# Kernel optimization log

Measured on AMD Instinct MI355X. Metric: run time of the kernel, lower is better.

Reference implementation:

```python
import jax, jax.numpy as jnp
import numpy as np

DIM = 2048
NUM_HEADS = 16
NUM_KV_HEADS = 4
HEAD_DIM = DIM // NUM_HEADS  # 128
ROPE_BASE = 10000.0
BATCH = 2
SEQLEN = 2048


def _rms_norm(x):
    # F.rms_norm over last dim, no weight; torch default eps = dtype eps
    eps = jnp.finfo(x.dtype).eps
    ms = jnp.mean(jnp.square(x), axis=-1, keepdims=True)
    return x * jax.lax.rsqrt(ms + eps)


def _rotary_cos_sin(seqlen, dtype):
    # Rotary(head_dim, base): inv_freq over even indices, freqs = t outer inv_freq
    inv_freq = 1.0 / (ROPE_BASE ** (jnp.arange(0, HEAD_DIM, 2, dtype=jnp.float32) / HEAD_DIM))
    t = jnp.arange(seqlen, dtype=jnp.float32)
    freqs = jnp.outer(t, inv_freq)  # [T, HEAD_DIM//2]
    return jnp.cos(freqs).astype(dtype), jnp.sin(freqs).astype(dtype)


def _apply_rotary_emb(x, cos, sin):
    # x: [B, H, T, D]; split halves (modded-nanogpt style)
    d = x.shape[-1] // 2
    x1, x2 = x[..., :d], x[..., d:]
    y1 = x1 * cos + x2 * sin
    y2 = -x1 * sin + x2 * cos
    return jnp.concatenate([y1, y2], axis=-1)


def setup_inputs() -> dict:
    key = jax.random.key(0)
    ks = jax.random.split(key, 6)
    kv_dim = NUM_KV_HEADS * HEAD_DIM
    s_in = 1.0 / np.sqrt(DIM)
    return {
        "x": jax.random.normal(ks[0], (BATCH, SEQLEN, DIM), dtype=jnp.float32),
        "q_gain": jax.random.uniform(ks[1], (NUM_HEADS,), dtype=jnp.float32, minval=0.5, maxval=1.5),
        "W_q": jax.random.normal(ks[2], (DIM, DIM), dtype=jnp.float32) * s_in,
        "W_k": jax.random.normal(ks[3], (kv_dim, DIM), dtype=jnp.float32) * s_in,
        "W_v": jax.random.normal(ks[4], (kv_dim, DIM), dtype=jnp.float32) * s_in,
        "W_proj": jax.random.normal(ks[5], (DIM, DIM), dtype=jnp.float32) * s_in,
    }


def reference(x, q_gain, W_q, W_k, W_v, W_proj):
    B, T, D = x.shape
    # QKV projections (Linear with weight [out, in])
    q = (x @ W_q.T).reshape(B, T, NUM_HEADS, HEAD_DIM).transpose(0, 2, 1, 3)   # [B,H,T,d]
    k = (x @ W_k.T).reshape(B, T, NUM_KV_HEADS, HEAD_DIM).transpose(0, 2, 1, 3)
    v = (x @ W_v.T).reshape(B, T, NUM_KV_HEADS, HEAD_DIM).transpose(0, 2, 1, 3)
    # dual RMSNorm on q/k
    q = _rms_norm(q)
    k = _rms_norm(k)
    # RoPE
    cos, sin = _rotary_cos_sin(T, q.dtype)
    q = _apply_rotary_emb(q, cos, sin)
    k = _apply_rotary_emb(k, cos, sin)
    # per-head gain on q
    q = q * q_gain.astype(q.dtype)[None, :, None, None]
    # GQA: repeat kv heads to match query heads
    g = NUM_HEADS // NUM_KV_HEADS
    k = jnp.repeat(k, g, axis=1)
    v = jnp.repeat(v, g, axis=1)
    # causal scaled dot product attention
    scale = 1.0 / np.sqrt(HEAD_DIM)
    scores = jnp.einsum('bhqd,bhkd->bhqk', q, k) * scale
    causal = jnp.tril(jnp.ones((T, T), dtype=bool))
    scores = jnp.where(causal[None, None], scores, jnp.finfo(scores.dtype).min)
    probs = jax.nn.softmax(scores, axis=-1)
    y = jnp.einsum('bhqk,bhkd->bhqd', probs, v)  # [B,H,T,d]
    y = y.transpose(0, 2, 1, 3).reshape(B, T, D)
    return y @ W_proj.T
```

## Files before the change

### kernel.cpp

```cpp
#include <hip/hip_runtime.h>
#include <hip/hip_bf16.h>
#include <type_traits>

#define DIMN   2048
#define NH     16
#define NKVH   4
#define HD     128
#define KVD    512
#define NQKV   3072
#define BATCH  2
#define SEQ    2048
#define MROWS  4096
#define VOFF   2560

typedef __attribute__((ext_vector_type(8))) __bf16 bf16x8;
typedef __attribute__((ext_vector_type(4))) float floatx4;

#define BIG_NEG (-1.0e30f)

__device__ __forceinline__ short bf16rn(float f) {
  union { __bf16 h; short s; } u;
  u.h = (__bf16)f;
  return u.s;
}
__device__ __forceinline__ float bf2f(short s) {
  union { unsigned u; float f; } v;
  v.u = ((unsigned)(unsigned short)s) << 16;
  return v.f;
}

__device__ __forceinline__ void async_cp16(const short* g, short* l) {
  __builtin_amdgcn_global_load_lds(
      (const __attribute__((address_space(1))) unsigned int*)g,
      (__attribute__((address_space(3))) unsigned int*)l, 16, 0, 0);
}

__global__ void f32_to_bf16_kern(const float* __restrict__ in,
                                 short* __restrict__ out, int n8) {
  int i = blockIdx.x * blockDim.x + threadIdx.x;
  if (i >= n8) return;
  float4 a = ((const float4*)in)[i * 2];
  float4 b = ((const float4*)in)[i * 2 + 1];
  short r[8];
  r[0] = bf16rn(a.x); r[1] = bf16rn(a.y); r[2] = bf16rn(a.z); r[3] = bf16rn(a.w);
  r[4] = bf16rn(b.x); r[5] = bf16rn(b.y); r[6] = bf16rn(b.z); r[7] = bf16rn(b.w);
  ((uint4*)out)[i] = *(const uint4*)r;
}

template <typename OUT>
__global__ __launch_bounds__(256) void gemm_bt_as(const short* __restrict__ A,
                                                  const short* __restrict__ Bw,
                                                  OUT* __restrict__ C,
                                                  int N, int K) {
  __shared__ __align__(16) short As[2][128 * 32];
  __shared__ __align__(16) short Bs[2][128 * 32];
  const int t = threadIdx.x;
  const int lane = t & 63, wave = t >> 6;
  const int lrow = lane & 15, quad = lane >> 4;
  const int wr = wave >> 1, wc = wave & 1;
  const int m0 = blockIdx.y * 128, n0 = blockIdx.x * 128;

  const short* pa[2];
  const short* pb[2];
  int wi2[2];
#pragma unroll
  for (int i = 0; i < 2; i++) {
    int wi = wave * 2 + i;
    int row = wi * 16 + (lane >> 2);
    int col = ((lane & 3) ^ (row & 3)) * 8;
    pa[i] = A + (size_t)(m0 + row) * K + col;
    pb[i] = Bw + (size_t)(n0 + row) * K + col;
    wi2[i] = wi;
  }

  floatx4 acc[4][4] = {};
  const int iters = K >> 5;

#pragma unroll
  for (int i = 0; i < 2; i++) {
    async_cp16(pa[i], &As[0][wi2[i] * 512]);
    async_cp16(pb[i], &Bs[0][wi2[i] * 512]);
  }

  for (int it = 0; it < iters; it++) {
    const int cur = it & 1;
    __syncthreads();

    if (it + 1 < iters) {
      const int off = (it + 1) * 32;
#pragma unroll
      for (int i = 0; i < 2; i++) {
        async_cp16(pa[i] + off, &As[cur ^ 1][wi2[i] * 512]);
        async_cp16(pb[i] + off, &Bs[cur ^ 1][wi2[i] * 512]);
      }
    }

    bf16x8 af[4], bfr[4];
#pragma unroll
    for (int mt = 0; mt < 4; mt++) {
      int row = wr * 64 + mt * 16 + lrow;
      af[mt] = *(const bf16x8*)&As[cur][row * 32 + (quad ^ (lrow & 3)) * 8];
    }
#pragma unroll
    for (int nt = 0; nt < 4; nt++) {
      int row = wc * 64 + nt * 16 + lrow;
      bfr[nt] = *(const bf16x8*)&Bs[cur][row * 32 + (quad ^ (lrow & 3)) * 8];
    }
#pragma unroll
    for (int mt = 0; mt < 4; mt++)
#pragma unroll
      for (int nt = 0; nt < 4; nt++)
        acc[mt][nt] = __builtin_amdgcn_mfma_f32_16x16x32_bf16(af[mt], bfr[nt],
                                                              acc[mt][nt], 0, 0, 0);
  }

#pragma unroll
  for (int mt = 0; mt < 4; mt++)
#pragma unroll
    for (int nt = 0; nt < 4; nt++) {
      int row = m0 + wr * 64 + mt * 16 + quad * 4;
      int col = n0 + wc * 64 + nt * 16 + lrow;
#pragma unroll
      for (int r = 0; r < 4; r++) {
        if constexpr (std::is_same<OUT, short>::value)
          C[(size_t)(row + r) * N + col] = bf16rn(acc[mt][nt][r]);
        else
          C[(size_t)(row + r) * N + col] = acc[mt][nt][r];
      }
    }
}

__global__ __launch_bounds__(256) void rms_rope_kern(const short* __restrict__ qkv,
                                                     const float* __restrict__ gain,
                                                     short* __restrict__ qb,
                                                     short* __restrict__ kb) {
  const int t = threadIdx.x;
  const int lane = t & 63, wave = t >> 6;
  const int gw = blockIdx.x * 4 + wave;
  const int row = gw / 20, slot = gw - row * 20;
  const int pos = row & (SEQ - 1);

  const short* src = (slot < 16) ? qkv + (size_t)row * NQKV + slot * HD
                                 : qkv + (size_t)row * NQKV + DIMN + (slot - 16) * HD;
  float x1 = bf2f(src[lane]), x2 = bf2f(src[lane + 64]);

  float ss = x1 * x1 + x2 * x2;
#pragma unroll
  for (int off = 32; off > 0; off >>= 1) ss += __shfl_xor(ss, off);
  float inv = rsqrtf(ss * (1.0f / 128.0f) + 1.1920928955078125e-7f);
  x1 *= inv; x2 *= inv;
  float fr = (float)pos * exp2f((float)lane * -0.20762050593045935f);
  float s, c;
  sincosf(fr, &s, &c);
  float y1 = x1 * c + x2 * s;
  float y2 = x2 * c - x1 * s;
  if (slot < 16) {
    float g = gain[slot] * 0.12751744459132754f;
    y1 *= g; y2 *= g;
  }
  short o1 = bf16rn(y1), o2 = bf16rn(y2);
  if (slot < 16) { short* d = qb + (size_t)row * DIMN + slot * HD;        d[lane] = o1; d[lane + 64] = o2; }
  else           { short* d = kb + (size_t)row * KVD + (slot - 16) * HD;  d[lane] = o1; d[lane + 64] = o2; }
}

__global__ __launch_bounds__(256) void vT_kern(const short* __restrict__ qkv,
                                               short* __restrict__ vT) {
  __shared__ short L[64 * 68];
  const int t0 = blockIdx.x * 64, d0 = blockIdx.y * 64;
  const int b = blockIdx.z >> 2, kvh = blockIdx.z & 3;
  const int t = threadIdx.x;

#pragma unroll
  for (int p = 0; p < 4; p++) {
    int tt = p * 16 + (t >> 4);
    int dd = (t & 15) * 4;
    ushort4 v = *(const ushort4*)(qkv + (size_t)(b * SEQ + t0 + tt) * NQKV + VOFF + kvh * HD + d0 + dd);
    *(ushort4*)&L[tt * 68 + dd] = v;
  }
  __syncthreads();

  const int dl = t >> 2;
  const int tc = (t & 3) * 16;
  short tmp[16];
#pragma unroll
  for (int j = 0; j < 16; j++) tmp[j] = L[(tc + j) * 68 + dl];
  size_t obase = (size_t)((b * NKVH + kvh) * HD + d0 + dl) * SEQ + t0 + tc;
  *(uint4*)(vT + obase)     = ((const uint4*)tmp)[0];
  *(uint4*)(vT + obase + 8) = ((const uint4*)tmp)[1];
}

__global__ __launch_bounds__(256) void attn_kern(const short* __restrict__ qb,
                                                 const short* __restrict__ kb,
                                                 const short* __restrict__ vT,
                                                 short* __restrict__ yb) {
  __shared__ __align__(16) short Ks[2][64 * 128];
  __shared__ __align__(16) short Vs[128 * 64];
  __shared__ __align__(16) short Ps[64 * 72];
  const int qp = blockIdx.x;
  const int g  = blockIdx.y;
  const int b = g >> 4, h = g & 15, kvh = h >> 2;
  const int t = threadIdx.x, lane = t & 63, wave = t >> 6;
  const int lrow = lane & 15, quad = lane >> 4;

  int k_row[4], k_col[4], v_row[4], v_col[4];
#pragma unroll
  for (int i = 0; i < 4; i++) {
    int wi = wave * 4 + i;
    int kr = wi * 4 + (lane >> 4);
    k_row[i] = kr; k_col[i] = ((lane & 15) ^ (kr & 7)) * 8;
    int vr = wi * 8 + (lane >> 3);
    v_row[i] = vr; v_col[i] = ((lane & 7) ^ (vr & 7)) * 8;
  }
  const short* kbase = kb + (size_t)b * SEQ * KVD + kvh * HD;
  const short* vbase = vT + (size_t)(b * NKVH + kvh) * HD * SEQ;

  bf16x8 vones;
#pragma unroll
  for (int j = 0; j < 8; j++) vones[j] = (__bf16)1.0f;

  for (int ph = 0; ph < 2; ph++) {
    const int qt = ph ? (31 - qp) : qp;
    const int q0 = qt * 64;

    __syncthreads();

    bf16x8 aq[4];
    const short* qrow = qb + (size_t)(b * SEQ + q0 + wave * 16 + lrow) * DIMN + h * HD;
#pragma unroll
    for (int kk = 0; kk < 4; kk++)
      aq[kk] = *(const bf16x8*)(qrow + kk * 32 + quad * 8);

    floatx4 O[8] = {};
    floatx4 Ol = {};
    float mI[4];
#pragma unroll
    for (int r = 0; r < 4; r++) mI[r] = BIG_NEG;

#pragma unroll
    for (int i = 0; i < 4; i++)
      async_cp16(kbase + (size_t)k_row[i] * KVD + k_col[i], &Ks[0][(wave * 4 + i) * 512]);

    for (int kt = 0; kt <= qt; kt++) {
      const int cur = kt & 1;
      const int k0 = kt * 64;
      __syncthreads();

#pragma unroll
      for (int i = 0; i < 4; i++)
        async_cp16(vbase + (size_t)v_row[i] * SEQ + k0 + v_col[i], &Vs[(wave * 4 + i) * 512]);
      if (kt < qt) {
        const int kn = k0 + 64;
#pragma unroll
        for (int i = 0; i < 4; i++)
          async_cp16(kbase + (size_t)(kn + k_row[i]) * KVD + k_col[i],
                     &Ks[cur ^ 1][(wave * 4 + i) * 512]);
      }

      floatx4 S[4] = {};
#pragma unroll
      for (int kk = 0; kk < 4; kk++)
#pragma unroll
        for (int nt = 0; nt < 4; nt++) {
          int row = nt * 16 + lrow;
          bf16x8 bk = *(const bf16x8*)&Ks[cur][row * 128 + ((kk * 4 + quad) ^ (row & 7)) * 8];
          S[nt] = __builtin_amdgcn_mfma_f32_16x16x32_bf16(aq[kk], bk, S[nt], 0, 0, 0);
        }

      if (kt == qt) {
#pragma unroll
        for (int nt = 0; nt < 4; nt++) {
          int kj = nt * 16 + lrow;
#pragma unroll
          for (int r = 0; r < 4; r++) {
            int qi = wave * 16 + quad * 4 + r;
            if (kj > qi) S[nt][r] = BIG_NEG;
          }
        }
      }

#pragma unroll
      for (int r = 0; r < 4; r++) {
        float mx = fmaxf(fmaxf(S[0][r], S[1][r]), fmaxf(S[2][r], S[3][r]));
        mx = fmaxf(mx, __shfl_xor(mx, 1));
        mx = fmaxf(mx, __shfl_xor(mx, 2));
        mx = fmaxf(mx, __shfl_xor(mx, 4));
        mx = fmaxf(mx, __shfl_xor(mx, 8));
        if (!__all(mx <= mI[r] + 8.0f)) {
          float mNew = fmaxf(mI[r], mx);
          float alpha = exp2f(mI[r] - mNew);
          mI[r] = mNew;
#pragma unroll
          for (int n2 = 0; n2 < 8; n2++) O[n2][r] *= alpha;
          Ol[r] *= alpha;
        }
#pragma unroll
        for (int nt = 0; nt < 4; nt++) S[nt][r] = exp2f(S[nt][r] - mI[r]);
      }

#pragma unroll
      for (int nt = 0; nt < 4; nt++) {
        int cwr = ((nt * 2 + (lrow >> 3)) ^ (quad * 2)) * 8 + (lrow & 7);
#pragma unroll
        for (int r = 0; r < 4; r++)
          Ps[(wave * 16 + quad * 4 + r) * 72 + cwr] = bf16rn(S[nt][r]);
      }

      __syncthreads();

#pragma unroll
      for (int kk = 0; kk < 2; kk++) {
        int capc = ((kk * 4 + quad) ^ (2 * ((lrow >> 2) & 3))) * 8;
        bf16x8 ap = *(const bf16x8*)&Ps[(wave * 16 + lrow) * 72 + capc];
#pragma unroll
        for (int n2 = 0; n2 < 8; n2++) {
          int row = n2 * 16 + lrow;
          bf16x8 bv = *(const bf16x8*)&Vs[row * 64 + ((kk * 4 + quad) ^ (row & 7)) * 8];
          O[n2] = __builtin_amdgcn_mfma_f32_16x16x32_bf16(ap, bv, O[n2], 0, 0, 0);
        }
        Ol = __builtin_amdgcn_mfma_f32_16x16x32_bf16(ap, vones, Ol, 0, 0, 0);
      }
    }

    float il[4];
#pragma unroll
    for (int r = 0; r < 4; r++) il[r] = 1.0f / Ol[r];
#pragma unroll
    for (int n2 = 0; n2 < 8; n2++)
#pragma unroll
      for (int r = 0; r < 4; r++) {
        float val = O[n2][r] * il[r];
        int row = q0 + wave * 16 + quad * 4 + r;
        int col = h * HD + n2 * 16 + lrow;
        yb[(size_t)(b * SEQ + row) * DIMN + col] = bf16rn(val);
      }
  }
}

extern "C" void kernel_launch(void* const* d_in, const int* in_sizes, int n_in,
                              void* d_out, int out_size, void* d_ws, size_t ws_size,
                              hipStream_t stream) {
  const float* x      = (const float*)d_in[0];
  const float* q_gain = (const float*)d_in[1];
  const float* W_q    = (const float*)d_in[2];
  const float* W_k    = (const float*)d_in[3];
  const float* W_v    = (const float*)d_in[4];
  const float* W_proj = (const float*)d_in[5];
  float* out = (float*)d_out;
  char* ws = (char*)d_ws;

  short* xb    = (short*)(ws);
  short* wqkv  = (short*)(ws + 16777216);
  short* wproj = (short*)(ws + 29360128);
  short* qkvb  = (short*)(ws + 37748736);
  short* q     = (short*)(ws + 62914560);
  short* k     = (short*)(ws + 79691776);
  short* vT    = (short*)(ws + 83886080);
  short* y     = xb;

  auto cvt = [&](const float* src, short* dst, int n) {
    int n8 = n / 8;
    f32_to_bf16_kern<<<(n8 + 255) / 256, 256, 0, stream>>>(src, dst, n8);
  };
  cvt(x, xb, MROWS * DIMN);
  cvt(W_q, wqkv, DIMN * DIMN);
  cvt(W_k, wqkv + DIMN * DIMN, KVD * DIMN);
  cvt(W_v, wqkv + DIMN * DIMN + KVD * DIMN, KVD * DIMN);
  cvt(W_proj, wproj, DIMN * DIMN);

  gemm_bt_as<short><<<dim3(NQKV / 128, MROWS / 128), 256, 0, stream>>>(xb, wqkv, qkvb, NQKV, DIMN);
  rms_rope_kern<<<(MROWS * 20) / 4, 256, 0, stream>>>(qkvb, q_gain, q, k);
  vT_kern<<<dim3(SEQ / 64, HD / 64, BATCH * NKVH), 256, 0, stream>>>(qkvb, vT);
  attn_kern<<<dim3(16, 32), 256, 0, stream>>>(q, k, vT, y);
  gemm_bt_as<float><<<dim3(DIMN / 128, MROWS / 128), 256, 0, stream>>>(y, wproj, out, DIMN, DIMN);
}
```

Baseline: 353.0 us.

## Use 128-row query tiles with 8 waves in attention and precompute RoPE table

The attention kernel moves from 64-query tiles with 4 waves, where each block handled a balanced pair of tiles, to 128-query tiles with 8 waves. Each K/V tile loaded into shared memory is now reused by twice as many query rows, and blocks are scheduled longest-first to reduce tail imbalance. A small kernel precomputes a cos/sin table into the scratch buffer so the RMS/RoPE kernel no longer calls sincos for every element. The costs are uneven work per block (no more pairing), an extra kernel launch, and a larger Ps buffer with a new stride of 64 instead of 72.

Result: slower. 409.4 us (+16.0%).

```diff
diff --git a/kernel.cpp b/kernel.cpp
--- a/kernel.cpp
+++ b/kernel.cpp
@@ -130,8 +130,18 @@
     }
 }
 
+__global__ void rope_tab_kern(float2* __restrict__ tab) {
+  int i = blockIdx.x * 256 + threadIdx.x;
+  int pos = i >> 6, ln = i & 63;
+  float fr = (float)pos * exp2f((float)ln * -0.20762050593045935f);
+  float s, c;
+  sincosf(fr, &s, &c);
+  tab[i] = make_float2(c, s);
+}
+
 __global__ __launch_bounds__(256) void rms_rope_kern(const short* __restrict__ qkv,
                                                      const float* __restrict__ gain,
+                                                     const float2* __restrict__ tab,
                                                      short* __restrict__ qb,
                                                      short* __restrict__ kb) {
   const int t = threadIdx.x;
@@ -149,9 +159,8 @@
   for (int off = 32; off > 0; off >>= 1) ss += __shfl_xor(ss, off);
   float inv = rsqrtf(ss * (1.0f / 128.0f) + 1.1920928955078125e-7f);
   x1 *= inv; x2 *= inv;
-  float fr = (float)pos * exp2f((float)lane * -0.20762050593045935f);
-  float s, c;
-  sincosf(fr, &s, &c);
+  float2 cs = tab[pos * 64 + lane];
+  float c = cs.x, s = cs.y;
   float y1 = x1 * c + x2 * s;
   float y2 = x2 * c - x1 * s;
   if (slot < 16) {
@@ -189,23 +198,25 @@
   *(uint4*)(vT + obase + 8) = ((const uint4*)tmp)[1];
 }
 
-__global__ __launch_bounds__(256) void attn_kern(const short* __restrict__ qb,
+__global__ __launch_bounds__(512) void attn_kern(const short* __restrict__ qb,
                                                  const short* __restrict__ kb,
                                                  const short* __restrict__ vT,
                                                  short* __restrict__ yb) {
   __shared__ __align__(16) short Ks[2][64 * 128];
   __shared__ __align__(16) short Vs[128 * 64];
-  __shared__ __align__(16) short Ps[64 * 72];
-  const int qp = blockIdx.x;
+  __shared__ __align__(16) short Ps[128 * 64];
+  const int qt = 15 - (int)blockIdx.x;
   const int g  = blockIdx.y;
   const int b = g >> 4, h = g & 15, kvh = h >> 2;
   const int t = threadIdx.x, lane = t & 63, wave = t >> 6;
   const int lrow = lane & 15, quad = lane >> 4;
-
-  int k_row[4], k_col[4], v_row[4], v_col[4];
-#pragma unroll
-  for (int i = 0; i < 4; i++) {
-    int wi = wave * 4 + i;
+  const int q0 = qt * 128;
+  const int KT = 2 * qt + 2;
+
+  int k_row[2], k_col[2], v_row[2], v_col[2];
+#pragma unroll
+  for (int i = 0; i < 2; i++) {
+    int wi = wave * 2 + i;
     int kr = wi * 4 + (lane >> 4);
     k_row[i] = kr; k_col[i] = ((lane & 15) ^ (kr & 7)) * 8;
     int vr = wi * 8 + (lane >> 3);
@@ -218,122 +229,115 @@
 #pragma unroll
   for (int j = 0; j < 8; j++) vones[j] = (__bf16)1.0f;
 
-  for (int ph = 0; ph < 2; ph++) {
-    const int qt = ph ? (31 - qp) : qp;
-    const int q0 = qt * 64;
-
+  bf16x8 aq[4];
+  const short* qrow = qb + (size_t)(b * SEQ + q0 + wave * 16 + lrow) * DIMN + h * HD;
+#pragma unroll
+  for (int kk = 0; kk < 4; kk++)
+    aq[kk] = *(const bf16x8*)(qrow + kk * 32 + quad * 8);
+
+  floatx4 O[8] = {};
+  floatx4 Ol = {};
+  float mI[4];
+#pragma unroll
+  for (int r = 0; r < 4; r++) mI[r] = BIG_NEG;
+
+#pragma unroll
+  for (int i = 0; i < 2; i++)
+    async_cp16(kbase + (size_t)k_row[i] * KVD + k_col[i], &Ks[0][(wave * 2 + i) * 512]);
+
+  for (int kt = 0; kt < KT; kt++) {
+    const int cur = kt & 1;
+    const int k0 = kt * 64;
     __syncthreads();
 
-    bf16x8 aq[4];
-    const short* qrow = qb + (size_t)(b * SEQ + q0 + wave * 16 + lrow) * DIMN + h * HD;
+#pragma unroll
+    for (int i = 0; i < 2; i++)
+      async_cp16(vbase + (size_t)v_row[i] * SEQ + k0 + v_col[i], &Vs[(wave * 2 + i) * 512]);
+    if (kt + 1 < KT) {
+      const int kn = k0 + 64;
+#pragma unroll
+      for (int i = 0; i < 2; i++)
+        async_cp16(kbase + (size_t)(kn + k_row[i]) * KVD + k_col[i],
+                   &Ks[cur ^ 1][(wave * 2 + i) * 512]);
+    }
+
+    floatx4 S[4] = {};
 #pragma unroll
     for (int kk = 0; kk < 4; kk++)
-      aq[kk] = *(const bf16x8*)(qrow + kk * 32 + quad * 8);
-
-    floatx4 O[8] = {};
-    floatx4 Ol = {};
-    float mI[4];
-#pragma unroll
-    for (int r = 0; r < 4; r++) mI[r] = BIG_NEG;
-
-#pragma unroll
-    for (int i = 0; i < 4; i++)
-      async_cp16(kbase + (size_t)k_row[i] * KVD + k_col[i], &Ks[0][(wave * 4 + i) * 512]);
-
-    for (int kt = 0; kt <= qt; kt++) {
-      const int cur = kt & 1;
-      const int k0 = kt * 64;
-      __syncthreads();
-
-#pragma unroll
-      for (int i = 0; i < 4; i++)
-        async_cp16(vbase + (size_t)v_row[i] * SEQ + k0 + v_col[i], &Vs[(wave * 4 + i) * 512]);
-      if (kt < qt) {
-        const int kn = k0 + 64;
-#pragma unroll
-        for (int i = 0; i < 4; i++)
-          async_cp16(kbase + (size_t)(kn + k_row[i]) * KVD + k_col[i],
-                     &Ks[cur ^ 1][(wave * 4 + i) * 512]);
-      }
-
-      floatx4 S[4] = {};
-#pragma unroll
-      for (int kk = 0; kk < 4; kk++)
-#pragma unroll
-        for (int nt = 0; nt < 4; nt++) {
-          int row = nt * 16 + lrow;
-          bf16x8 bk = *(const bf16x8*)&Ks[cur][row * 128 + ((kk * 4 + quad) ^ (row & 7)) * 8];
-          S[nt] = __builtin_amdgcn_mfma_f32_16x16x32_bf16(aq[kk], bk, S[nt], 0, 0, 0);
+#pragma unroll
+      for (int nt = 0; nt < 4; nt++) {
+        int row = nt * 16 + lrow;
+        bf16x8 bk = *(const bf16x8*)&Ks[cur][row * 128 + ((kk * 4 + quad) ^ (row & 7)) * 8];
+        S[nt] = __builtin_amdgcn_mfma_f32_16x16x32_bf16(aq[kk], bk, S[nt], 0, 0, 0);
+      }
+
+    if (kt >= 2 * qt) {
+#pragma unroll
+      for (int nt = 0; nt < 4; nt++) {
+        int kglob = k0 + nt * 16 + lrow;
+#pragma unroll
+        for (int r = 0; r < 4; r++) {
+          int qglob = q0 + wave * 16 + quad * 4 + r;
+          if (kglob > qglob) S[nt][r] = BIG_NEG;
         }
-
-      if (kt == qt) {
-#pragma unroll
-        for (int nt = 0; nt < 4; nt++) {
-          int kj = nt * 16 + lrow;
-#pragma unroll
-          for (int r = 0; r < 4; r++) {
-            int qi = wave * 16 + quad * 4 + r;
-            if (kj > qi) S[nt][r] = BIG_NEG;
-          }
-        }
-      }
-
-#pragma unroll
-      for (int r = 0; r < 4; r++) {
-        float mx = fmaxf(fmaxf(S[0][r], S[1][r]), fmaxf(S[2][r], S[3][r]));
-        mx = fmaxf(mx, __shfl_xor(mx, 1));
-        mx = fmaxf(mx, __shfl_xor(mx, 2));
-        mx = fmaxf(mx, __shfl_xor(mx, 4));
-        mx = fmaxf(mx, __shfl_xor(mx, 8));
-        if (!__all(mx <= mI[r] + 8.0f)) {
-          float mNew = fmaxf(mI[r], mx);
-          float alpha = exp2f(mI[r] - mNew);
-          mI[r] = mNew;
-#pragma unroll
-          for (int n2 = 0; n2 < 8; n2++) O[n2][r] *= alpha;
-          Ol[r] *= alpha;
-        }
-#pragma unroll
-        for (int nt = 0; nt < 4; nt++) S[nt][r] = exp2f(S[nt][r] - mI[r]);
-      }
-
-#pragma unroll
-      for (int nt = 0; nt < 4; nt++) {
-        int cwr = ((nt * 2 + (lrow >> 3)) ^ (quad * 2)) * 8 + (lrow & 7);
-#pragma unroll
-        for (int r = 0; r < 4; r++)
-          Ps[(wave * 16 + quad * 4 + r) * 72 + cwr] = bf16rn(S[nt][r]);
-      }
-
-      __syncthreads();
-
-#pragma unroll
-      for (int kk = 0; kk < 2; kk++) {
-        int capc = ((kk * 4 + quad) ^ (2 * ((lrow >> 2) & 3))) * 8;
-        bf16x8 ap = *(const bf16x8*)&Ps[(wave * 16 + lrow) * 72 + capc];
-#pragma unroll
-        for (int n2 = 0; n2 < 8; n2++) {
-          int row = n2 * 16 + lrow;
-          bf16x8 bv = *(const bf16x8*)&Vs[row * 64 + ((kk * 4 + quad) ^ (row & 7)) * 8];
-          O[n2] = __builtin_amdgcn_mfma_f32_16x16x32_bf16(ap, bv, O[n2], 0, 0, 0);
-        }
-        Ol = __builtin_amdgcn_mfma_f32_16x16x32_bf16(ap, vones, Ol, 0, 0, 0);
-      }
-    }
-
-    float il[4];
-#pragma unroll
-    for (int r = 0; r < 4; r++) il[r] = 1.0f / Ol[r];
-#pragma unroll
-    for (int n2 = 0; n2 < 8; n2++)
-#pragma unroll
-      for (int r = 0; r < 4; r++) {
-        float val = O[n2][r] * il[r];
-        int row = q0 + wave * 16 + quad * 4 + r;
-        int col = h * HD + n2 * 16 + lrow;
-        yb[(size_t)(b * SEQ + row) * DIMN + col] = bf16rn(val);
-      }
-  }
+      }
+    }
+
+#pragma unroll
+    for (int r = 0; r < 4; r++) {
+      float mx = fmaxf(fmaxf(S[0][r], S[1][r]), fmaxf(S[2][r], S[3][r]));
+      mx = fmaxf(mx, __shfl_xor(mx, 1));
+      mx = fmaxf(mx, __shfl_xor(mx, 2));
+      mx = fmaxf(mx, __shfl_xor(mx, 4));
+      mx = fmaxf(mx, __shfl_xor(mx, 8));
+      if (!__all(mx <= mI[r] + 8.0f)) {
+        float mNew = fmaxf(mI[r], mx);
+        float alpha = exp2f(mI[r] - mNew);
+        mI[r] = mNew;
+#pragma unroll
+        for (int n2 = 0; n2 < 8; n2++) O[n2][r] *= alpha;
+        Ol[r] *= alpha;
+      }
+#pragma unroll
+      for (int nt = 0; nt < 4; nt++) S[nt][r] = exp2f(S[nt][r] - mI[r]);
+    }
+
+#pragma unroll
+    for (int nt = 0; nt < 4; nt++) {
+      int cwr = ((nt * 2 + (lrow >> 3)) ^ (quad * 2)) * 8 + (lrow & 7);
+#pragma unroll
+      for (int r = 0; r < 4; r++)
+        Ps[(wave * 16 + quad * 4 + r) * 64 + cwr] = bf16rn(S[nt][r]);
+    }
+
+    __syncthreads();
+
+#pragma unroll
+    for (int kk = 0; kk < 2; kk++) {
+      int capc = ((kk * 4 + quad) ^ (2 * ((lrow >> 2) & 3))) * 8;
+      bf16x8 ap = *(const bf16x8*)&Ps[(wave * 16 + lrow) * 64 + capc];
+#pragma unroll
+      for (int n2 = 0; n2 < 8; n2++) {
+        int row = n2 * 16 + lrow;
+        bf16x8 bv = *(const bf16x8*)&Vs[row * 64 + ((kk * 4 + quad) ^ (row & 7)) * 8];
+        O[n2] = __builtin_amdgcn_mfma_f32_16x16x32_bf16(ap, bv, O[n2], 0, 0, 0);
+      }
+      Ol = __builtin_amdgcn_mfma_f32_16x16x32_bf16(ap, vones, Ol, 0, 0, 0);
+    }
+  }
+
+  float il[4];
+#pragma unroll
+  for (int r = 0; r < 4; r++) il[r] = 1.0f / Ol[r];
+#pragma unroll
+  for (int n2 = 0; n2 < 8; n2++)
+#pragma unroll
+    for (int r = 0; r < 4; r++) {
+      float val = O[n2][r] * il[r];
+      int row = q0 + wave * 16 + quad * 4 + r;
+      int col = h * HD + n2 * 16 + lrow;
+      yb[(size_t)(b * SEQ + row) * DIMN + col] = bf16rn(val);
+    }
 }
 
 extern "C" void kernel_launch(void* const* d_in, const int* in_sizes, int n_in,
@@ -356,6 +360,7 @@
   short* k     = (short*)(ws + 79691776);
   short* vT    = (short*)(ws + 83886080);
   short* y     = xb;
+  float2* tab  = (float2*)xb;
 
   auto cvt = [&](const float* src, short* dst, int n) {
     int n8 = n / 8;
@@ -368,8 +373,9 @@
   cvt(W_proj, wproj, DIMN * DIMN);
 
   gemm_bt_as<short><<<dim3(NQKV / 128, MROWS / 128), 256, 0, stream>>>(xb, wqkv, qkvb, NQKV, DIMN);
-  rms_rope_kern<<<(MROWS * 20) / 4, 256, 0, stream>>>(qkvb, q_gain, q, k);
+  rope_tab_kern<<<(SEQ * 64) / 256, 256, 0, stream>>>(tab);
+  rms_rope_kern<<<(MROWS * 20) / 4, 256, 0, stream>>>(qkvb, q_gain, tab, q, k);
   vT_kern<<<dim3(SEQ / 64, HD / 64, BATCH * NKVH), 256, 0, stream>>>(qkvb, vT);
-  attn_kern<<<dim3(16, 32), 256, 0, stream>>>(q, k, vT, y);
+  attn_kern<<<dim3(16, 32), 512, 0, stream>>>(q, k, vT, y);
   gemm_bt_as<float><<<dim3(DIMN / 128, MROWS / 128), 256, 0, stream>>>(y, wproj, out, DIMN, DIMN);
 }
```

## Transpose attention MFMA operands and precompute RoPE cos/sin table

Applied to the files above, without the earlier changes.

The attention kernel now swaps MFMA operand order so each lane owns a single query row. Row max and rescale then take two cross-lane shuffles instead of four per row, and only one running max is kept. P is packed as bf16 pairs into a swizzled word layout, and output rows are written as contiguous 8-byte stores. Separately, RoPE cos/sin values are computed once into a table that reuses the xb workspace after the QKV GEMM, instead of calling sincosf per element. This adds one small kernel launch and per-element table reads.

Result: faster. 323.4 us (-8.4%).

```diff
diff --git a/kernel.cpp b/kernel.cpp
--- a/kernel.cpp
+++ b/kernel.cpp
@@ -27,6 +27,10 @@
   union { unsigned u; float f; } v;
   v.u = ((unsigned)(unsigned short)s) << 16;
   return v.f;
+}
+__device__ __forceinline__ unsigned pack2bf(float a, float b) {
+  return (unsigned)(unsigned short)bf16rn(a) |
+         ((unsigned)(unsigned short)bf16rn(b) << 16);
 }
 
 __device__ __forceinline__ void async_cp16(const short* g, short* l) {
@@ -130,8 +134,18 @@
     }
 }
 
+__global__ void rope_tab_kern(float2* __restrict__ tab) {
+  int i = blockIdx.x * 256 + threadIdx.x;
+  int pos = i >> 6, ln = i & 63;
+  float fr = (float)pos * exp2f((float)ln * -0.20762050593045935f);
+  float s, c;
+  sincosf(fr, &s, &c);
+  tab[i] = make_float2(c, s);
+}
+
 __global__ __launch_bounds__(256) void rms_rope_kern(const short* __restrict__ qkv,
                                                      const float* __restrict__ gain,
+                                                     const float2* __restrict__ tab,
                                                      short* __restrict__ qb,
                                                      short* __restrict__ kb) {
   const int t = threadIdx.x;
@@ -149,9 +163,8 @@
   for (int off = 32; off > 0; off >>= 1) ss += __shfl_xor(ss, off);
   float inv = rsqrtf(ss * (1.0f / 128.0f) + 1.1920928955078125e-7f);
   x1 *= inv; x2 *= inv;
-  float fr = (float)pos * exp2f((float)lane * -0.20762050593045935f);
-  float s, c;
-  sincosf(fr, &s, &c);
+  float2 cs = tab[pos * 64 + lane];
+  float c = cs.x, s = cs.y;
   float y1 = x1 * c + x2 * s;
   float y2 = x2 * c - x1 * s;
   if (slot < 16) {
@@ -195,12 +208,13 @@
                                                  short* __restrict__ yb) {
   __shared__ __align__(16) short Ks[2][64 * 128];
   __shared__ __align__(16) short Vs[128 * 64];
-  __shared__ __align__(16) short Ps[64 * 72];
+  __shared__ __align__(16) unsigned Psw[64 * 32];
   const int qp = blockIdx.x;
   const int g  = blockIdx.y;
   const int b = g >> 4, h = g & 15, kvh = h >> 2;
   const int t = threadIdx.x, lane = t & 63, wave = t >> 6;
   const int lrow = lane & 15, quad = lane >> 4;
+  const int qrow = wave * 16 + lrow;
 
   int k_row[4], k_col[4], v_row[4], v_col[4];
 #pragma unroll
@@ -225,16 +239,14 @@
     __syncthreads();
 
     bf16x8 aq[4];
-    const short* qrow = qb + (size_t)(b * SEQ + q0 + wave * 16 + lrow) * DIMN + h * HD;
+    const short* qrw = qb + (size_t)(b * SEQ + q0 + qrow) * DIMN + h * HD;
 #pragma unroll
     for (int kk = 0; kk < 4; kk++)
-      aq[kk] = *(const bf16x8*)(qrow + kk * 32 + quad * 8);
+      aq[kk] = *(const bf16x8*)(qrw + kk * 32 + quad * 8);
 
     floatx4 O[8] = {};
     floatx4 Ol = {};
-    float mI[4];
-#pragma unroll
-    for (int r = 0; r < 4; r++) mI[r] = BIG_NEG;
+    float mI = BIG_NEG;
 
 #pragma unroll
     for (int i = 0; i < 4; i++)
@@ -256,83 +268,84 @@
                      &Ks[cur ^ 1][(wave * 4 + i) * 512]);
       }
 
-      floatx4 S[4] = {};
+      floatx4 St[4] = {};
 #pragma unroll
       for (int kk = 0; kk < 4; kk++)
 #pragma unroll
         for (int nt = 0; nt < 4; nt++) {
           int row = nt * 16 + lrow;
           bf16x8 bk = *(const bf16x8*)&Ks[cur][row * 128 + ((kk * 4 + quad) ^ (row & 7)) * 8];
-          S[nt] = __builtin_amdgcn_mfma_f32_16x16x32_bf16(aq[kk], bk, S[nt], 0, 0, 0);
+          St[nt] = __builtin_amdgcn_mfma_f32_16x16x32_bf16(bk, aq[kk], St[nt], 0, 0, 0);
         }
 
       if (kt == qt) {
 #pragma unroll
-        for (int nt = 0; nt < 4; nt++) {
-          int kj = nt * 16 + lrow;
+        for (int nt = 0; nt < 4; nt++)
 #pragma unroll
           for (int r = 0; r < 4; r++) {
-            int qi = wave * 16 + quad * 4 + r;
-            if (kj > qi) S[nt][r] = BIG_NEG;
+            int kj = nt * 16 + quad * 4 + r;
+            if (kj > qrow) St[nt][r] = BIG_NEG;
           }
+      }
+
+      float mx = St[0][0];
+#pragma unroll
+      for (int nt = 0; nt < 4; nt++)
+#pragma unroll
+        for (int r = 0; r < 4; r++) mx = fmaxf(mx, St[nt][r]);
+      mx = fmaxf(mx, __shfl_xor(mx, 16));
+      mx = fmaxf(mx, __shfl_xor(mx, 32));
+      if (!__all(mx <= mI + 8.0f)) {
+        float mNew = fmaxf(mI, mx);
+        float alpha = exp2f(mI - mNew);
+        mI = mNew;
+#pragma unroll
+        for (int n2 = 0; n2 < 8; n2++) O[n2] *= alpha;
+        Ol *= alpha;
+      }
+#pragma unroll
+      for (int nt = 0; nt < 4; nt++)
+#pragma unroll
+        for (int r = 0; r < 4; r++) St[nt][r] = exp2f(St[nt][r] - mI);
+
+#pragma unroll
+      for (int nt = 0; nt < 4; nt++)
+#pragma unroll
+        for (int hh = 0; hh < 2; hh++) {
+          int kw = nt * 8 + quad * 2 + hh;
+          Psw[qrow * 32 + (kw ^ lrow ^ (((kw >> 3) & 1) << 4))] =
+              pack2bf(St[nt][2 * hh], St[nt][2 * hh + 1]);
         }
-      }
-
-#pragma unroll
-      for (int r = 0; r < 4; r++) {
-        float mx = fmaxf(fmaxf(S[0][r], S[1][r]), fmaxf(S[2][r], S[3][r]));
-        mx = fmaxf(mx, __shfl_xor(mx, 1));
-        mx = fmaxf(mx, __shfl_xor(mx, 2));
-        mx = fmaxf(mx, __shfl_xor(mx, 4));
-        mx = fmaxf(mx, __shfl_xor(mx, 8));
-        if (!__all(mx <= mI[r] + 8.0f)) {
-          float mNew = fmaxf(mI[r], mx);
-          float alpha = exp2f(mI[r] - mNew);
-          mI[r] = mNew;
-#pragma unroll
-          for (int n2 = 0; n2 < 8; n2++) O[n2][r] *= alpha;
-          Ol[r] *= alpha;
+
+      __syncthreads();
+
+#pragma unroll
+      for (int kk = 0; kk < 2; kk++) {
+        union { unsigned u[4]; bf16x8 v; } bp;
+#pragma unroll
+        for (int j2 = 0; j2 < 4; j2++) {
+          int kw = kk * 16 + quad * 4 + j2;
+          bp.u[j2] = Psw[qrow * 32 + (kw ^ lrow ^ (((kw >> 3) & 1) << 4))];
         }
-#pragma unroll
-        for (int nt = 0; nt < 4; nt++) S[nt][r] = exp2f(S[nt][r] - mI[r]);
-      }
-
-#pragma unroll
-      for (int nt = 0; nt < 4; nt++) {
-        int cwr = ((nt * 2 + (lrow >> 3)) ^ (quad * 2)) * 8 + (lrow & 7);
-#pragma unroll
-        for (int r = 0; r < 4; r++)
-          Ps[(wave * 16 + quad * 4 + r) * 72 + cwr] = bf16rn(S[nt][r]);
-      }
-
-      __syncthreads();
-
-#pragma unroll
-      for (int kk = 0; kk < 2; kk++) {
-        int capc = ((kk * 4 + quad) ^ (2 * ((lrow >> 2) & 3))) * 8;
-        bf16x8 ap = *(const bf16x8*)&Ps[(wave * 16 + lrow) * 72 + capc];
 #pragma unroll
         for (int n2 = 0; n2 < 8; n2++) {
           int row = n2 * 16 + lrow;
           bf16x8 bv = *(const bf16x8*)&Vs[row * 64 + ((kk * 4 + quad) ^ (row & 7)) * 8];
-          O[n2] = __builtin_amdgcn_mfma_f32_16x16x32_bf16(ap, bv, O[n2], 0, 0, 0);
+          O[n2] = __builtin_amdgcn_mfma_f32_16x16x32_bf16(bv, bp.v, O[n2], 0, 0, 0);
         }
-        Ol = __builtin_amdgcn_mfma_f32_16x16x32_bf16(ap, vones, Ol, 0, 0, 0);
-      }
-    }
-
-    float il[4];
-#pragma unroll
-    for (int r = 0; r < 4; r++) il[r] = 1.0f / Ol[r];
-#pragma unroll
-    for (int n2 = 0; n2 < 8; n2++)
-#pragma unroll
-      for (int r = 0; r < 4; r++) {
-        float val = O[n2][r] * il[r];
-        int row = q0 + wave * 16 + quad * 4 + r;
-        int col = h * HD + n2 * 16 + lrow;
-        yb[(size_t)(b * SEQ + row) * DIMN + col] = bf16rn(val);
-      }
+        Ol = __builtin_amdgcn_mfma_f32_16x16x32_bf16(vones, bp.v, Ol, 0, 0, 0);
+      }
+    }
+
+    float il = 1.0f / Ol[0];
+    short* yrow = yb + (size_t)(b * SEQ + q0 + qrow) * DIMN + h * HD;
+#pragma unroll
+    for (int n2 = 0; n2 < 8; n2++) {
+      short o[4];
+#pragma unroll
+      for (int r = 0; r < 4; r++) o[r] = bf16rn(O[n2][r] * il);
+      *(uint2*)&yrow[n2 * 16 + quad * 4] = *(const uint2*)o;
+    }
   }
 }
 
@@ -356,6 +369,7 @@
   short* k     = (short*)(ws + 79691776);
   short* vT    = (short*)(ws + 83886080);
   short* y     = xb;
+  float2* tab  = (float2*)xb;
 
   auto cvt = [&](const float* src, short* dst, int n) {
     int n8 = n / 8;
@@ -368,7 +382,8 @@
   cvt(W_proj, wproj, DIMN * DIMN);
 
   gemm_bt_as<short><<<dim3(NQKV / 128, MROWS / 128), 256, 0, stream>>>(xb, wqkv, qkvb, NQKV, DIMN);
-  rms_rope_kern<<<(MROWS * 20) / 4, 256, 0, stream>>>(qkvb, q_gain, q, k);
+  rope_tab_kern<<<(SEQ * 64) / 256, 256, 0, stream>>>(tab);
+  rms_rope_kern<<<(MROWS * 20) / 4, 256, 0, stream>>>(qkvb, q_gain, tab, q, k);
   vT_kern<<<dim3(SEQ / 64, HD / 64, BATCH * NKVH), 256, 0, stream>>>(qkvb, vT);
   attn_kern<<<dim3(16, 32), 256, 0, stream>>>(q, k, vT, y);
   gemm_bt_as<float><<<dim3(DIMN / 128, MROWS / 128), 256, 0, stream>>>(y, wproj, out, DIMN, DIMN);
```
